# Optimization experiments

Measured on AMD Instinct MI355X. Metric: run time of the kernel, lower is better.

## Reference

```python
import jax, jax.numpy as jnp
import numpy as np

B, S, D, H, E = 4, 2048, 1024, 4096, 8
TOP_K = 2


def setup_inputs() -> dict:
    key = jax.random.key(0)
    k = jax.random.split(key, 7)
    scale_in = 1.0 / np.sqrt(D)
    scale_h = 1.0 / np.sqrt(H)
    return {
        "x": jax.random.normal(k[0], (B, S, D), jnp.float32),
        "Wr": jax.random.normal(k[1], (D, E), jnp.float32) * scale_in,
        "br": jnp.zeros((E,), jnp.float32),
        "W1": jax.random.normal(k[2], (E, D, H), jnp.float32) * scale_in,
        "b1": jnp.zeros((E, H), jnp.float32),
        "W2": jax.random.normal(k[3], (E, H, D), jnp.float32) * scale_h,
        "b2": jnp.zeros((E, D), jnp.float32),
    }


def reference(x, Wr, br, W1, b1, W2, b2):
    # Router: softmax over experts, then top-k and renormalize.
    routing = jax.nn.softmax(x @ Wr + br, axis=-1)            # [B,S,E]
    topk_vals, topk_idx = jax.lax.top_k(routing, TOP_K)        # [B,S,K]
    topk_norm = topk_vals / jnp.sum(topk_vals, axis=-1, keepdims=True)
    # Scatter normalized top-k weights back to a dense [B,S,E] gate.
    gate = jnp.sum(jax.nn.one_hot(topk_idx, E, dtype=x.dtype) * topk_norm[..., None], axis=2)  # [B,S,E]
    # Per-expert FFN over all tokens (original's dense masked loop; masked-out
    # tokens have gate==0 so zeroing inputs is mathematically equivalent).
    h = jax.nn.relu(jnp.einsum("bsd,edh->ebsh", x, W1) + b1[:, None, None, :])  # [E,B,S,H]
    y = jnp.einsum("ebsh,ehd->ebsd", h, W2) + b2[:, None, None, :]              # [E,B,S,D]
    out = jnp.einsum("ebsd,bse->bsd", y, gate)                                   # [B,S,D]
    return out
```

## Files before the change

### kernel.cpp

```cpp
#include <hip/hip_runtime.h>
#include <stdint.h>

typedef unsigned short u16;
typedef __attribute__((ext_vector_type(8))) short s8bf;
typedef __attribute__((ext_vector_type(4))) float f32x4;

#define N_TOK 8192
#define DIM   1024
#define HID   4096
#define NE    8
#define MAX_SLOTS 17408
#define MAX_TILES 160
#define TSTR  264

#define OFF_W1T  ((size_t)0)
#define OFF_Y    ((size_t)0)
#define OFF_W2T  ((size_t)67108864)
#define OFF_XB   ((size_t)134217728)
#define OFF_H    ((size_t)150994944)
#define OFF_TOS  ((size_t)293601280)
#define OFF_SOT  ((size_t)293670912)
#define OFF_TKI  ((size_t)293740544)
#define OFF_TKW  ((size_t)293806080)
#define OFF_CNT  ((size_t)293871616)
#define OFF_POF  ((size_t)293871680)
#define OFF_CUR  ((size_t)293871744)
#define OFF_NT   ((size_t)293871808)
#define OFF_TE   ((size_t)293871872)
#define OFF_TS   ((size_t)293872896)

__device__ __forceinline__ u16 f2b(float v) {
  union { float f; uint32_t u; } c; c.f = v;
  uint32_t u = c.u;
  return (u16)((u + 0x7FFFu + ((u >> 16) & 1u)) >> 16);
}
__device__ __forceinline__ float b2f(u16 b) {
  union { uint32_t u; float f; } c; c.u = ((uint32_t)b) << 16; return c.f;
}

typedef const __attribute__((address_space(1))) uint32_t* gp32;
typedef __attribute__((address_space(3))) uint32_t* lp32;
__device__ __forceinline__ void gl_lds16(const u16* g, u16* l) {
  __builtin_amdgcn_global_load_lds((gp32)(const void*)g, (lp32)(void*)l, 16, 0, 0);
}

__global__ __launch_bounds__(256) void transpose_to_bf16(
    const float* __restrict__ in, u16* __restrict__ out, int R, int C) {
  __shared__ u16 L[64 * TSTR];
  int tiles_c = C >> 6, tiles_r = R >> 8;
  int per = tiles_c * tiles_r;
  int e = blockIdx.x / per, t = blockIdx.x % per;
  int tr = t / tiles_c, tc = t % tiles_c;
  const float* ip = in + (size_t)e * R * C + (size_t)(tr * 256) * C + tc * 64;
  u16* op = out + (size_t)e * R * C + (size_t)(tc * 64) * R + tr * 256;
  const int tid = threadIdx.x;
  const int c = tid & 63;
  const int rb0 = (tid >> 6) * 8;
  #pragma unroll
  for (int p = 0; p < 8; p++) {
    int rb = p * 32 + rb0;
    u16 tmp[8];
    #pragma unroll
    for (int j = 0; j < 8; j++) tmp[j] = f2b(ip[(size_t)(rb + j) * C + c]);
    *(uint4*)&L[c * TSTR + rb] = *(const uint4*)tmp;
  }
  __syncthreads();
  const int s = tid & 31, ocb = tid >> 5;
  #pragma unroll
  for (int p = 0; p < 8; p++) {
    int oc = p * 8 + ocb;
    uint4 v = *(const uint4*)&L[oc * TSTR + s * 8];
    *(uint4*)&op[(size_t)oc * R + s * 8] = v;
  }
}

__global__ __launch_bounds__(256) void convert_x(const float* __restrict__ x,
                                                 u16* __restrict__ xb) {
  size_t i = ((size_t)blockIdx.x * 256 + threadIdx.x) * 8;
  float4 v0 = *(const float4*)(x + i);
  float4 v1 = *(const float4*)(x + i + 4);
  u16 o[8] = {f2b(v0.x), f2b(v0.y), f2b(v0.z), f2b(v0.w),
              f2b(v1.x), f2b(v1.y), f2b(v1.z), f2b(v1.w)};
  *(uint4*)(xb + i) = *(const uint4*)o;
}

__global__ __launch_bounds__(256) void router_kernel(
    const float* __restrict__ x, const float* __restrict__ Wr,
    const float* __restrict__ br, int* __restrict__ tki, float* __restrict__ tkw,
    int* __restrict__ counts) {
  int wave = threadIdx.x >> 6, lane = threadIdx.x & 63;
  int t = blockIdx.x * 4 + wave;
  const float* xr = x + (size_t)t * DIM;
  float acc[8] = {0.f, 0.f, 0.f, 0.f, 0.f, 0.f, 0.f, 0.f};
  #pragma unroll
  for (int i = 0; i < 16; i++) {
    int d = lane + i * 64;
    float xv = xr[d];
    float4 wa = *(const float4*)(Wr + d * 8);
    float4 wb = *(const float4*)(Wr + d * 8 + 4);
    acc[0] += xv * wa.x; acc[1] += xv * wa.y; acc[2] += xv * wa.z; acc[3] += xv * wa.w;
    acc[4] += xv * wb.x; acc[5] += xv * wb.y; acc[6] += xv * wb.z; acc[7] += xv * wb.w;
  }
  #pragma unroll
  for (int e = 0; e < 8; e++)
    #pragma unroll
    for (int off = 32; off >= 1; off >>= 1)
      acc[e] += __shfl_xor(acc[e], off, 64);
  if (lane == 0) {
    float l[8];
    #pragma unroll
    for (int e = 0; e < 8; e++) l[e] = acc[e] + br[e];
    float l0 = -1e30f; int i0 = 0;
    #pragma unroll
    for (int e = 0; e < 8; e++) if (l[e] > l0) { l0 = l[e]; i0 = e; }
    float l1 = -1e30f; int i1 = 0;
    #pragma unroll
    for (int e = 0; e < 8; e++) if (e != i0 && l[e] > l1) { l1 = l[e]; i1 = e; }
    float w0 = 1.f / (1.f + expf(l1 - l0));
    tki[t * 2] = i0; tki[t * 2 + 1] = i1;
    tkw[t * 2] = w0; tkw[t * 2 + 1] = 1.f - w0;
    atomicAdd(&counts[i0], 1);
    atomicAdd(&counts[i1], 1);
  }
}

__global__ void plan_kernel(const int* __restrict__ counts, int* __restrict__ poff,
                            int* __restrict__ cursor, int* __restrict__ ntiles,
                            int* __restrict__ tile_e, int* __restrict__ tile_s0) {
  int e = threadIdx.x;
  if (e < NE) {
    int po = 0, tb = 0;
    for (int i = 0; i < e; i++) {
      int tl = (counts[i] + 127) >> 7;
      po += tl << 7; tb += tl;
    }
    poff[e] = po;
    cursor[e] = 0;
    int tl = (counts[e] + 127) >> 7;
    for (int j = 0; j < tl; j++) { tile_e[tb + j] = e; tile_s0[tb + j] = po + j * 128; }
    if (e == NE - 1) ntiles[0] = tb + tl;
  }
}

__global__ __launch_bounds__(256) void scatter_kernel(
    const int* __restrict__ tki, const int* __restrict__ poff,
    int* __restrict__ cursor, int* __restrict__ token_of_slot,
    int* __restrict__ slot_of_token) {
  int t = blockIdx.x * 256 + threadIdx.x;
  #pragma unroll
  for (int k = 0; k < 2; k++) {
    int e = tki[t * 2 + k];
    int r = atomicAdd(&cursor[e], 1);
    int s = poff[e] + r;
    token_of_slot[s] = t;
    slot_of_token[t * 2 + k] = s;
  }
}

template <int MODE>
__global__ __launch_bounds__(512, 2) void moe_gemm(
    const u16* __restrict__ A, const u16* __restrict__ Bt,
    const float* __restrict__ bias, u16* __restrict__ Hout,
    const int* __restrict__ tile_e, const int* __restrict__ tile_s0,
    const int* __restrict__ ntiles, const int* __restrict__ token_of_slot,
    int K, int N, int NB) {
  __shared__ u16 SM[49152];

  const int nblk = blockIdx.x % NB;
  const int tileid = blockIdx.x / NB;
  if (tileid >= ntiles[0]) return;
  const int e = tile_e[tileid];
  const int slot0 = tile_s0[tileid];
  const int n0 = nblk * 256;
  const int T = K >> 6;

  const int tid = threadIdx.x;
  const int lane = tid & 63;
  const int wave = tid >> 6;
  const int wm = wave >> 2;
  const int wn = wave & 3;

  const int srow = tid >> 3;
  const int sslot = tid & 7;
  const u16* aB[2];
  #pragma unroll
  for (int l = 0; l < 2; l++) {
    int row = l * 64 + srow;
    int scol = (sslot ^ (row & 7)) * 8;
    int arow;
    if (MODE == 1) { int t0 = token_of_slot[slot0 + row]; arow = t0 < 0 ? 0 : t0; }
    else arow = slot0 + row;
    aB[l] = A + (size_t)arow * K + scol;
  }
  const u16* bE = Bt + (size_t)e * N * K;
  const u16* bB[4];
  #pragma unroll
  for (int l = 0; l < 4; l++) {
    int row = l * 64 + srow;
    int scol = (sslot ^ (row & 7)) * 8;
    bB[l] = bE + (size_t)(n0 + row) * K + scol;
  }

  const int colq = lane & 15;
  float bv[4];
  #pragma unroll
  for (int n = 0; n < 4; n++) bv[n] = bias[(size_t)e * N + n0 + wn * 64 + n * 16 + colq];
  asm volatile("s_waitcnt vmcnt(0)" ::: "memory");

  const int wb = wave * 64;
  #pragma unroll
  for (int tt = 0; tt < 2; tt++) {
    const int kq = tt * 64;
    u16* LA = SM + tt * 8192;
    u16* LB = SM + 16384 + tt * 16384;
    gl_lds16(aB[0] + kq, LA + wb * 8);
    gl_lds16(aB[1] + kq, LA + (512 + wb) * 8);
    gl_lds16(bB[0] + kq, LB + wb * 8);
    gl_lds16(bB[1] + kq, LB + (512 + wb) * 8);
    gl_lds16(bB[2] + kq, LB + (1024 + wb) * 8);
    gl_lds16(bB[3] + kq, LB + (1536 + wb) * 8);
  }
  asm volatile("s_waitcnt vmcnt(6)" ::: "memory");
  __builtin_amdgcn_s_barrier();

  const int q4 = lane >> 4;
  const int sx = lane & 7;
  const int sk0 = (q4 ^ sx) * 8;
  const int sk1 = sk0 ^ 32;
  const int aOff = (wm * 64 + (lane & 15)) * 64;
  const int bOff = (wn * 64 + (lane & 15)) * 64;

  f32x4 acc[4][4];
  #pragma unroll
  for (int i = 0; i < 4; i++)
    #pragma unroll
    for (int j = 0; j < 4; j++) acc[i][j] = (f32x4){0.f, 0.f, 0.f, 0.f};

  int kk = 128;
  for (int t = 0; t < T; ++t) {
    const int cb = t & 1;
    const u16* LA = SM + cb * 8192;
    const u16* LB = SM + 16384 + cb * 16384;
    u16* sLA = SM + cb * 8192;
    u16* sLB = SM + 16384 + cb * 16384;
    s8bf af[4][2], bf[4][2];

    #pragma unroll
    for (int m = 0; m < 4; m++) {
      af[m][0] = *(const s8bf*)&LA[aOff + m * 1024 + sk0];
      af[m][1] = *(const s8bf*)&LA[aOff + m * 1024 + sk1];
    }
    #pragma unroll
    for (int n = 0; n < 2; n++) {
      bf[n][0] = *(const s8bf*)&LB[bOff + n * 1024 + sk0];
      bf[n][1] = *(const s8bf*)&LB[bOff + n * 1024 + sk1];
    }
    __builtin_amdgcn_sched_barrier(0);
    __builtin_amdgcn_s_barrier();
    __builtin_amdgcn_s_setprio(1);
    #pragma unroll
    for (int ks = 0; ks < 2; ks++)
      #pragma unroll
      for (int m = 0; m < 4; m++)
        #pragma unroll
        for (int n = 0; n < 2; n++)
          acc[m][n] = __builtin_amdgcn_mfma_f32_16x16x32_bf16(af[m][ks], bf[n][ks],
                                                              acc[m][n], 0, 0, 0);
    __builtin_amdgcn_s_setprio(0);
    __builtin_amdgcn_s_barrier();

    #pragma unroll
    for (int n = 2; n < 4; n++) {
      bf[n][0] = *(const s8bf*)&LB[bOff + n * 1024 + sk0];
      bf[n][1] = *(const s8bf*)&LB[bOff + n * 1024 + sk1];
    }
    __builtin_amdgcn_sched_barrier(0);
    __builtin_amdgcn_s_barrier();
    __builtin_amdgcn_s_setprio(1);
    #pragma unroll
    for (int ks = 0; ks < 2; ks++)
      #pragma unroll
      for (int m = 0; m < 4; m++)
        #pragma unroll
        for (int n = 2; n < 4; n++)
          acc[m][n] = __builtin_amdgcn_mfma_f32_16x16x32_bf16(af[m][ks], bf[n][ks],
                                                              acc[m][n], 0, 0, 0);
    __builtin_amdgcn_s_setprio(0);
    asm volatile("s_waitcnt lgkmcnt(0)" ::: "memory");
    __builtin_amdgcn_sched_barrier(0);
    __builtin_amdgcn_s_barrier();

    if (t + 2 < T) {
      gl_lds16(aB[0] + kk, sLA + wb * 8);
      gl_lds16(aB[1] + kk, sLA + (512 + wb) * 8);
      gl_lds16(bB[0] + kk, sLB + wb * 8);
      gl_lds16(bB[1] + kk, sLB + (512 + wb) * 8);
      gl_lds16(bB[2] + kk, sLB + (1024 + wb) * 8);
      gl_lds16(bB[3] + kk, sLB + (1536 + wb) * 8);
    }
    __builtin_amdgcn_sched_barrier(0);
    if (t < T - 2)       asm volatile("s_waitcnt vmcnt(6)" ::: "memory");
    else if (t == T - 2) asm volatile("s_waitcnt vmcnt(0)" ::: "memory");
    if (t < T - 1) {
      __builtin_amdgcn_sched_barrier(0);
      __builtin_amdgcn_s_barrier();
    }
    kk += 64;
  }

  #pragma unroll
  for (int m = 0; m < 4; m++) {
    __syncthreads();
    const int rbase = wm * 16 + ((lane >> 4) << 2);
    #pragma unroll
    for (int n = 0; n < 4; n++) {
      const int lcol = wn * 64 + n * 16 + colq;
      #pragma unroll
      for (int r = 0; r < 4; r++) {
        float v = acc[m][n][r] + bv[n];
        if (MODE == 1) v = fmaxf(v, 0.f);
        SM[(rbase + r) * 264 + lcol] = f2b(v);
      }
    }
    __syncthreads();
    #pragma unroll
    for (int it = 0; it < 2; it++) {
      const int idx = it * 512 + tid;
      const int rl = idx >> 5;
      const int c16 = (idx & 31) * 8;
      const int grow = (rl < 16) ? (m * 16 + rl) : (48 + m * 16 + rl);
      uint4 v = *(const uint4*)&SM[rl * 264 + c16];
      *(uint4*)&Hout[(size_t)(slot0 + grow) * N + n0 + c16] = v;
    }
  }
}

__global__ __launch_bounds__(256) void combine_kernel(
    const u16* __restrict__ y, const int* __restrict__ sot,
    const float* __restrict__ tkw, float* __restrict__ out) {
  int wave = threadIdx.x >> 6, lane = threadIdx.x & 63;
  int t = blockIdx.x * 4 + wave;
  int s0 = sot[t * 2], s1 = sot[t * 2 + 1];
  float w0 = tkw[t * 2], w1 = tkw[t * 2 + 1];
  const u16* y0 = y + (size_t)s0 * DIM;
  const u16* y1 = y + (size_t)s1 * DIM;
  float* op = out + (size_t)t * DIM;
  #pragma unroll
  for (int i = 0; i < 4; i++) {
    int d = i * 256 + lane * 4;
    uint2 a = *(const uint2*)(y0 + d);
    uint2 b = *(const uint2*)(y1 + d);
    float4 o;
    o.x = w0 * b2f((u16)(a.x & 0xFFFF)) + w1 * b2f((u16)(b.x & 0xFFFF));
    o.y = w0 * b2f((u16)(a.x >> 16))    + w1 * b2f((u16)(b.x >> 16));
    o.z = w0 * b2f((u16)(a.y & 0xFFFF)) + w1 * b2f((u16)(b.y & 0xFFFF));
    o.w = w0 * b2f((u16)(a.y >> 16))    + w1 * b2f((u16)(b.y >> 16));
    *(float4*)(op + d) = o;
  }
}

extern "C" void kernel_launch(void* const* d_in, const int* in_sizes, int n_in,
                              void* d_out, int out_size, void* d_ws, size_t ws_size,
                              hipStream_t stream) {
  const float* x  = (const float*)d_in[0];
  const float* Wr = (const float*)d_in[1];
  const float* br = (const float*)d_in[2];
  const float* W1 = (const float*)d_in[3];
  const float* b1 = (const float*)d_in[4];
  const float* W2 = (const float*)d_in[5];
  const float* b2 = (const float*)d_in[6];
  float* out = (float*)d_out;
  char* ws = (char*)d_ws;

  u16*   W1t  = (u16*)(ws + OFF_W1T);
  u16*   W2t  = (u16*)(ws + OFF_W2T);
  u16*   ybuf = (u16*)(ws + OFF_Y);
  u16*   xb   = (u16*)(ws + OFF_XB);
  u16*   hbuf = (u16*)(ws + OFF_H);
  int*   tos  = (int*)(ws + OFF_TOS);
  int*   sot  = (int*)(ws + OFF_SOT);
  int*   tki  = (int*)(ws + OFF_TKI);
  float* tkw  = (float*)(ws + OFF_TKW);
  int*   cnt  = (int*)(ws + OFF_CNT);
  int*   pof  = (int*)(ws + OFF_POF);
  int*   cur  = (int*)(ws + OFF_CUR);
  int*   nt   = (int*)(ws + OFF_NT);
  int*   te   = (int*)(ws + OFF_TE);
  int*   ts   = (int*)(ws + OFF_TS);

  hipMemsetAsync(tos, 0xFF, (size_t)MAX_SLOTS * sizeof(int), stream);
  hipMemsetAsync(cnt, 0, 8 * sizeof(int), stream);

  transpose_to_bf16<<<dim3(NE * (DIM / 256) * (HID / 64)), 256, 0, stream>>>(W1, W1t, DIM, HID);
  transpose_to_bf16<<<dim3(NE * (HID / 256) * (DIM / 64)), 256, 0, stream>>>(W2, W2t, HID, DIM);
  convert_x<<<dim3(N_TOK * DIM / (256 * 8)), 256, 0, stream>>>(x, xb);
  router_kernel<<<dim3(N_TOK / 4), 256, 0, stream>>>(x, Wr, br, tki, tkw, cnt);
  plan_kernel<<<dim3(1), 64, 0, stream>>>(cnt, pof, cur, nt, te, ts);
  scatter_kernel<<<dim3(N_TOK / 256), 256, 0, stream>>>(tki, pof, cur, tos, sot);

  moe_gemm<1><<<dim3((MAX_SLOTS / 128) * (HID / 256)), 512, 0, stream>>>(
      xb, W1t, b1, hbuf, te, ts, nt, tos, DIM, HID, HID / 256);
  moe_gemm<2><<<dim3((MAX_SLOTS / 128) * (DIM / 256)), 512, 0, stream>>>(
      hbuf, W2t, b2, ybuf, te, ts, nt, tos, HID, DIM, DIM / 256);
  combine_kernel<<<dim3(N_TOK / 4), 256, 0, stream>>>(ybuf, sot, tkw, out);
}
```

Measured before the change: 1.048 ms.

## Shrink MoE GEMM tile to 128x128 with 256-thread blocks

The grouped expert GEMM moves from a 128x256 output tile with 8 waves to a 128x128 tile with 4 waves, each wave still computing a 64x64 subtile. Shared memory drops to 64KB, the load staging is reorganised into four 32-row slabs per operand, and the epilogue writes the whole tile to LDS in one pass instead of four row chunks. The aim is more blocks and better occupancy or load balance on the padded token tiles. The cost is lower reuse of the A operand per block and more global traffic for B.

```diff
diff --git a/kernel.cpp b/kernel.cpp
--- a/kernel.cpp
+++ b/kernel.cpp
@@ -12,6 +12,7 @@
 #define MAX_SLOTS 17408
 #define MAX_TILES 160
 #define TSTR  264
+#define LSTR  152
 
 #define OFF_W1T  ((size_t)0)
 #define OFF_Y    ((size_t)0)
@@ -158,47 +159,47 @@
 }
 
 template <int MODE>
-__global__ __launch_bounds__(512, 2) void moe_gemm(
+__global__ __launch_bounds__(256, 2) void moe_gemm(
     const u16* __restrict__ A, const u16* __restrict__ Bt,
     const float* __restrict__ bias, u16* __restrict__ Hout,
     const int* __restrict__ tile_e, const int* __restrict__ tile_s0,
     const int* __restrict__ ntiles, const int* __restrict__ token_of_slot,
     int K, int N, int NB) {
-  __shared__ u16 SM[49152];
+  __shared__ u16 SM[32768];
 
   const int nblk = blockIdx.x % NB;
   const int tileid = blockIdx.x / NB;
   if (tileid >= ntiles[0]) return;
   const int e = tile_e[tileid];
   const int slot0 = tile_s0[tileid];
-  const int n0 = nblk * 256;
+  const int n0 = nblk * 128;
   const int T = K >> 6;
 
   const int tid = threadIdx.x;
   const int lane = tid & 63;
   const int wave = tid >> 6;
-  const int wm = wave >> 2;
-  const int wn = wave & 3;
+  const int wm = wave >> 1;
+  const int wn = wave & 1;
 
   const int srow = tid >> 3;
   const int sslot = tid & 7;
-  const u16* aB[2];
-  #pragma unroll
-  for (int l = 0; l < 2; l++) {
-    int row = l * 64 + srow;
+  const u16* aB[4];
+  const u16* bB[4];
+  #pragma unroll
+  for (int s = 0; s < 4; s++) {
+    int row = s * 32 + srow;
     int scol = (sslot ^ (row & 7)) * 8;
     int arow;
     if (MODE == 1) { int t0 = token_of_slot[slot0 + row]; arow = t0 < 0 ? 0 : t0; }
     else arow = slot0 + row;
-    aB[l] = A + (size_t)arow * K + scol;
+    aB[s] = A + (size_t)arow * K + scol;
   }
   const u16* bE = Bt + (size_t)e * N * K;
-  const u16* bB[4];
-  #pragma unroll
-  for (int l = 0; l < 4; l++) {
-    int row = l * 64 + srow;
+  #pragma unroll
+  for (int s = 0; s < 4; s++) {
+    int row = s * 32 + srow;
     int scol = (sslot ^ (row & 7)) * 8;
-    bB[l] = bE + (size_t)(n0 + row) * K + scol;
+    bB[s] = bE + (size_t)(n0 + row) * K + scol;
   }
 
   const int colq = lane & 15;
@@ -207,20 +208,18 @@
   for (int n = 0; n < 4; n++) bv[n] = bias[(size_t)e * N + n0 + wn * 64 + n * 16 + colq];
   asm volatile("s_waitcnt vmcnt(0)" ::: "memory");
 
-  const int wb = wave * 64;
+  const int wo = wave * 512;
   #pragma unroll
   for (int tt = 0; tt < 2; tt++) {
     const int kq = tt * 64;
     u16* LA = SM + tt * 8192;
-    u16* LB = SM + 16384 + tt * 16384;
-    gl_lds16(aB[0] + kq, LA + wb * 8);
-    gl_lds16(aB[1] + kq, LA + (512 + wb) * 8);
-    gl_lds16(bB[0] + kq, LB + wb * 8);
-    gl_lds16(bB[1] + kq, LB + (512 + wb) * 8);
-    gl_lds16(bB[2] + kq, LB + (1024 + wb) * 8);
-    gl_lds16(bB[3] + kq, LB + (1536 + wb) * 8);
-  }
-  asm volatile("s_waitcnt vmcnt(6)" ::: "memory");
+    u16* LB = SM + 16384 + tt * 8192;
+    #pragma unroll
+    for (int s = 0; s < 4; s++) gl_lds16(aB[s] + kq, LA + s * 2048 + wo);
+    #pragma unroll
+    for (int s = 0; s < 4; s++) gl_lds16(bB[s] + kq, LB + s * 2048 + wo);
+  }
+  asm volatile("s_waitcnt vmcnt(8)" ::: "memory");
   __builtin_amdgcn_s_barrier();
 
   const int q4 = lane >> 4;
@@ -240,9 +239,9 @@
   for (int t = 0; t < T; ++t) {
     const int cb = t & 1;
     const u16* LA = SM + cb * 8192;
-    const u16* LB = SM + 16384 + cb * 16384;
+    const u16* LB = SM + 16384 + cb * 8192;
     u16* sLA = SM + cb * 8192;
-    u16* sLB = SM + 16384 + cb * 16384;
+    u16* sLB = SM + 16384 + cb * 8192;
     s8bf af[4][2], bf[4][2];
 
     #pragma unroll
@@ -291,15 +290,13 @@
     __builtin_amdgcn_s_barrier();
 
     if (t + 2 < T) {
-      gl_lds16(aB[0] + kk, sLA + wb * 8);
-      gl_lds16(aB[1] + kk, sLA + (512 + wb) * 8);
-      gl_lds16(bB[0] + kk, sLB + wb * 8);
-      gl_lds16(bB[1] + kk, sLB + (512 + wb) * 8);
-      gl_lds16(bB[2] + kk, sLB + (1024 + wb) * 8);
-      gl_lds16(bB[3] + kk, sLB + (1536 + wb) * 8);
+      #pragma unroll
+      for (int s = 0; s < 4; s++) gl_lds16(aB[s] + kk, sLA + s * 2048 + wo);
+      #pragma unroll
+      for (int s = 0; s < 4; s++) gl_lds16(bB[s] + kk, sLB + s * 2048 + wo);
     }
     __builtin_amdgcn_sched_barrier(0);
-    if (t < T - 2)       asm volatile("s_waitcnt vmcnt(6)" ::: "memory");
+    if (t < T - 2)       asm volatile("s_waitcnt vmcnt(8)" ::: "memory");
     else if (t == T - 2) asm volatile("s_waitcnt vmcnt(0)" ::: "memory");
     if (t < T - 1) {
       __builtin_amdgcn_sched_barrier(0);
@@ -308,30 +305,30 @@
     kk += 64;
   }
 
-  #pragma unroll
-  for (int m = 0; m < 4; m++) {
-    __syncthreads();
-    const int rbase = wm * 16 + ((lane >> 4) << 2);
-    #pragma unroll
-    for (int n = 0; n < 4; n++) {
-      const int lcol = wn * 64 + n * 16 + colq;
+  __syncthreads();
+  const int rq = (lane >> 4) * 4;
+  #pragma unroll
+  for (int nt = 0; nt < 4; nt++) {
+    int lcol = wn * 64 + nt * 16 + colq;
+    #pragma unroll
+    for (int mt = 0; mt < 4; mt++) {
+      int rowbase = wm * 64 + mt * 16 + rq;
       #pragma unroll
       for (int r = 0; r < 4; r++) {
-        float v = acc[m][n][r] + bv[n];
+        float v = acc[mt][nt][r] + bv[nt];
         if (MODE == 1) v = fmaxf(v, 0.f);
-        SM[(rbase + r) * 264 + lcol] = f2b(v);
+        SM[(rowbase + r) * LSTR + lcol] = f2b(v);
       }
     }
-    __syncthreads();
-    #pragma unroll
-    for (int it = 0; it < 2; it++) {
-      const int idx = it * 512 + tid;
-      const int rl = idx >> 5;
-      const int c16 = (idx & 31) * 8;
-      const int grow = (rl < 16) ? (m * 16 + rl) : (48 + m * 16 + rl);
-      uint4 v = *(const uint4*)&SM[rl * 264 + c16];
-      *(uint4*)&Hout[(size_t)(slot0 + grow) * N + n0 + c16] = v;
-    }
+  }
+  __syncthreads();
+  #pragma unroll
+  for (int k = 0; k < 8; k++) {
+    int ch = k * 256 + tid;
+    int row = ch >> 4;
+    int cp = (ch & 15) * 8;
+    uint4 v = *(const uint4*)&SM[row * LSTR + cp];
+    *(uint4*)&Hout[(size_t)(slot0 + row) * N + n0 + cp] = v;
   }
 }
 
@@ -398,9 +395,9 @@
   plan_kernel<<<dim3(1), 64, 0, stream>>>(cnt, pof, cur, nt, te, ts);
   scatter_kernel<<<dim3(N_TOK / 256), 256, 0, stream>>>(tki, pof, cur, tos, sot);
 
-  moe_gemm<1><<<dim3((MAX_SLOTS / 128) * (HID / 256)), 512, 0, stream>>>(
-      xb, W1t, b1, hbuf, te, ts, nt, tos, DIM, HID, HID / 256);
-  moe_gemm<2><<<dim3((MAX_SLOTS / 128) * (DIM / 256)), 512, 0, stream>>>(
-      hbuf, W2t, b2, ybuf, te, ts, nt, tos, HID, DIM, DIM / 256);
+  moe_gemm<1><<<dim3((MAX_SLOTS / 128) * (HID / 128)), 256, 0, stream>>>(
+      xb, W1t, b1, hbuf, te, ts, nt, tos, DIM, HID, HID / 128);
+  moe_gemm<2><<<dim3((MAX_SLOTS / 128) * (DIM / 128)), 256, 0, stream>>>(
+      hbuf, W2t, b2, ybuf, te, ts, nt, tos, HID, DIM, DIM / 128);
   combine_kernel<<<dim3(N_TOK / 4), 256, 0, stream>>>(ybuf, sot, tkw, out);
 }
```

Measured after the change: 959.4 us. 8.5% less time.
